# Kernel tuning notes

Hardware: AMD Instinct MI355X
Metric: run time of the kernel (lower is better)

## Reference

```python
import jax, jax.numpy as jnp
import numpy as np

B, L, H, V = 256, 4096, 64, 64
LN_EPS = 1e-5


def setup_inputs() -> dict:
    key = jax.random.key(0)
    ks = jax.random.split(key, 12)
    s = 1.0 / np.sqrt(H)
    return {
        "seq": jax.random.randint(ks[0], (B, L), 0, V),
        "embed_W": jax.random.normal(ks[1], (V, H), jnp.float32),
        "ff_w1": jax.random.normal(ks[2], (H, 2 * H), jnp.float32) * s,
        "ff_b1": jnp.zeros((2 * H,), jnp.float32),
        "ff_w2": jax.random.normal(ks[3], (2 * H, H), jnp.float32) * s,
        "ff_b2": jnp.zeros((H,), jnp.float32),
        "ln_w": jnp.ones((H,), jnp.float32),
        "ln_b": jnp.zeros((H,), jnp.float32),
        "read_w": jax.random.normal(ks[4], (H, H), jnp.float32) * s,
        "read_b": jnp.zeros((H,), jnp.float32),
        "out_w": jax.random.normal(ks[5], (H, V), jnp.float32) * s,
        "out_b": jnp.zeros((V,), jnp.float32),
    }


def _layer_norm(x, w, b):
    mu = jnp.mean(x, axis=-1, keepdims=True)
    var = jnp.mean(jnp.square(x - mu), axis=-1, keepdims=True)
    return (x - mu) * jax.lax.rsqrt(var + LN_EPS) * w + b


def reference(seq, embed_W, ff_w1, ff_b1, ff_w2, ff_b2, ln_w, ln_b,
              read_w, read_b, out_w, out_b):
    h = embed_W[seq]  # (B, L, H)
    ff = jax.nn.relu(h @ ff_w1 + ff_b1) @ ff_w2 + ff_b2
    h = _layer_norm(h + ff, ln_w, ln_b)

    def step(M, k):  # M: (B,H,H), k: (B,H)
        v_pred = jnp.einsum('bij,bj->bi', M, k)
        denom = jnp.sum(k * k, axis=-1, keepdims=True) + 1e-6
        dv = k - v_pred / denom
        M = M + dv[:, :, None] * k[:, None, :]  # rank-1 delta write
        return M, None

    ks = jnp.swapaxes(h[:, :-1, :], 0, 1)  # (L-1, B, H)
    M0 = jnp.zeros((h.shape[0], h.shape[-1], h.shape[-1]), h.dtype)
    M, _ = jax.lax.scan(step, M0, ks)

    q = h[:, -1, :]
    ctx = jnp.einsum('bij,bj->bi', M, q)
    return (ctx @ read_w + read_b) @ out_w + out_b  # (B, V)
```

## Files before the change

### kernel.cpp

```cpp
#include <hip/hip_runtime.h>
#include <hip/hip_bf16.h>

#define LN_EPS 1e-5f

static __device__ __forceinline__ float readlane_f(float v, int lane) {
    return __int_as_float(__builtin_amdgcn_readlane(__float_as_int(v), lane));
}
static __device__ __forceinline__ void writelane_f(int& dst, float val, int lane_imm) {
    asm volatile("v_writelane_b32 %0, %1, %2"
                 : "+v"(dst)
                 : "s"(__float_as_int(val)), "i"(lane_imm));
}

__global__ __launch_bounds__(64) void build_keys(
    const float* __restrict__ embed,
    const float* __restrict__ w1,
    const float* __restrict__ b1,
    const float* __restrict__ w2,
    const float* __restrict__ b2,
    const float* __restrict__ lnw,
    const float* __restrict__ lnb,
    float* __restrict__ keytab)
{
    const int v = blockIdx.x, lane = threadIdx.x;
    __shared__ float se[64];
    __shared__ float sh[128];
    se[lane] = embed[v * 64 + lane];
    __syncthreads();
    float h0 = b1[lane];
    float h1 = b1[lane + 64];
    #pragma unroll 8
    for (int i = 0; i < 64; ++i) {
        float e = se[i];
        h0 = fmaf(e, w1[i * 128 + lane], h0);
        h1 = fmaf(e, w1[i * 128 + lane + 64], h1);
    }
    sh[lane]      = fmaxf(h0, 0.f);
    sh[lane + 64] = fmaxf(h1, 0.f);
    __syncthreads();
    float acc = b2[lane];
    #pragma unroll 8
    for (int j = 0; j < 128; ++j)
        acc = fmaf(sh[j], w2[j * 64 + lane], acc);
    float pre = se[lane] + acc;
    float sum = pre;
    #pragma unroll
    for (int off = 32; off >= 1; off >>= 1) sum += __shfl_xor(sum, off, 64);
    float mu  = sum * (1.f / 64.f);
    float dev = pre - mu;
    float sq  = dev * dev;
    #pragma unroll
    for (int off = 32; off >= 1; off >>= 1) sq += __shfl_xor(sq, off, 64);
    float var = sq * (1.f / 64.f);
    float key = dev * (1.f / sqrtf(var + LN_EPS)) * lnw[lane] + lnb[lane];
    keytab[v * 64 + lane] = key;
}

__global__ __launch_bounds__(64) void build_tables(
    const float* __restrict__ keytab,
    const float* __restrict__ read_w,
    const float* __restrict__ read_b,
    const float* __restrict__ out_w,
    const float* __restrict__ out_b,
    float* __restrict__ Gg,
    float* __restrict__ GhatN,
    float* __restrict__ Wc,
    float* __restrict__ biasv)
{
    const int w = blockIdx.x, lane = threadIdx.x;
    __shared__ float sk[64 * 65];
    __shared__ float srw[64];
    #pragma unroll 8
    for (int r = 0; r < 64; ++r) sk[r * 65 + lane] = keytab[r * 64 + lane];
    srw[lane] = read_w[w * 64 + lane];
    __syncthreads();
    float g = 0.f;
    #pragma unroll 8
    for (int i = 0; i < 64; ++i)
        g = fmaf(sk[w * 65 + i], sk[lane * 65 + i], g);
    float gww  = readlane_f(g, w);
    float beta = 1.f / (gww + 1e-6f);
    Gg[w * 64 + lane]    = g;
    GhatN[w * 64 + lane] = -(beta * g);
    float acc = 0.f;
    #pragma unroll 8
    for (int j = 0; j < 64; ++j)
        acc = fmaf(srw[j], out_w[j * 64 + lane], acc);
    Wc[w * 64 + lane] = acc;
    if (w == 0) {
        float bacc = out_b[lane];
        #pragma unroll 8
        for (int j = 0; j < 64; ++j)
            bacc = fmaf(read_b[j], out_w[j * 64 + lane], bacc);
        biasv[lane] = bacc;
    }
}

__global__ __launch_bounds__(64) void delta_scan(
    const int*   __restrict__ seq,
    const float* __restrict__ Gg,
    const float* __restrict__ GhatN,
    const float* __restrict__ keytab,
    const float* __restrict__ Wc,
    const float* __restrict__ biasv,
    float* __restrict__ out)
{
    const int lane = threadIdx.x;
    const int b    = blockIdx.x;
    __shared__ float sG[64 * 64];
    __shared__ float sc[64];
    __shared__ float sCtx[64];
    #pragma unroll 8
    for (int r = 0; r < 64; ++r) sG[r * 64 + lane] = GhatN[r * 64 + lane];
    sc[lane] = 0.f;
    const int* seqb = seq + (size_t)b * 4096;
    float d = Gg[seqb[4095] * 64 + lane];
    __syncthreads();

    int vS = 0;
    int vcur = seqb[64 * 63 + lane];
    int   wq[21];
    float q_[21];
    #pragma unroll
    for (int s = 0; s < 21; ++s) {
        wq[s] = __builtin_amdgcn_readlane(vcur, 62 - s);
        q_[s] = sG[wq[s] * 64 + lane];
    }

    #pragma unroll 1
    for (int blk = 64; blk >= 0; --blk) {
        int vnext = (blk > 0) ? seqb[(blk - 1) * 63 + lane] : vcur;
        #pragma unroll
        for (int j = 62; j >= 0; --j) {
            const int slot = (62 - j) % 21;
            const int jl   = j - 21;
            int   w0 = wq[slot];
            float p  = readlane_f(d, w0);
            d = fmaf(p, q_[slot], d);
            writelane_f(vS, p, j);
            int wn = (jl >= 0) ? __builtin_amdgcn_readlane(vcur, jl)
                               : __builtin_amdgcn_readlane(vnext, jl + 63);
            wq[slot] = wn;
            q_[slot] = sG[wn * 64 + lane];
        }
        atomicAdd(&sc[vcur & 63], __int_as_float(vS));
        vS = 0;
        vcur = vnext;
    }
    __syncthreads();

    float ctx = 0.f;
    #pragma unroll 8
    for (int v = 0; v < 64; ++v)
        ctx = fmaf(sc[v], keytab[v * 64 + lane], ctx);
    sCtx[lane] = ctx;
    __syncthreads();
    float o = biasv[lane];
    #pragma unroll 8
    for (int i = 0; i < 64; ++i)
        o = fmaf(sCtx[i], Wc[i * 64 + lane], o);
    out[(size_t)b * 64 + lane] = o;
}

extern "C" void kernel_launch(void* const* d_in, const int* in_sizes, int n_in,
                              void* d_out, int out_size, void* d_ws, size_t ws_size,
                              hipStream_t stream) {
    const int*   seq    = (const int*)d_in[0];
    const float* embed  = (const float*)d_in[1];
    const float* ff_w1  = (const float*)d_in[2];
    const float* ff_b1  = (const float*)d_in[3];
    const float* ff_w2  = (const float*)d_in[4];
    const float* ff_b2  = (const float*)d_in[5];
    const float* ln_w   = (const float*)d_in[6];
    const float* ln_b   = (const float*)d_in[7];
    const float* read_w = (const float*)d_in[8];
    const float* read_b = (const float*)d_in[9];
    const float* out_w  = (const float*)d_in[10];
    const float* out_b  = (const float*)d_in[11];
    float* out = (float*)d_out;

    float* wsf    = (float*)d_ws;
    float* keytab = wsf;
    float* Gg     = wsf + 4096;
    float* GhatN  = wsf + 8192;
    float* Wc     = wsf + 12288;
    float* biasv  = wsf + 16384;

    build_keys<<<64, 64, 0, stream>>>(embed, ff_w1, ff_b1, ff_w2, ff_b2, ln_w, ln_b, keytab);
    build_tables<<<64, 64, 0, stream>>>(keytab, read_w, read_b, out_w, out_b,
                                        Gg, GhatN, Wc, biasv);
    delta_scan<<<256, 64, 0, stream>>>(seq, Gg, GhatN, keytab, Wc, biasv, out);
}
```

Baseline: 167.3 us.

## Pair scan steps algebraically and read Gram rows from global memory instead of LDS

The serial delta-scan recurrence now processes two steps per iteration. The second step's readlane is computed from the first step's value plus a precomputed cross term, which shortens the dependent chain of readlane and fma per step. The shared-memory copy of the normalized Gram table is removed, and rows are fetched straight from global memory (likely L1/L2-resident). This trades the LDS preload and its latency for global loads, and adds one extra readlane plus readfirstlane per pair.

```diff
diff --git a/kernel.cpp b/kernel.cpp
--- a/kernel.cpp
+++ b/kernel.cpp
@@ -10,6 +10,12 @@
     asm volatile("v_writelane_b32 %0, %1, %2"
                  : "+v"(dst)
                  : "s"(__float_as_int(val)), "i"(lane_imm));
+}
+static __device__ __forceinline__ void writelane_fu(int& dst, float val, int lane_imm) {
+    int sval = __builtin_amdgcn_readfirstlane(__float_as_int(val));
+    asm volatile("v_writelane_b32 %0, %1, %2"
+                 : "+v"(dst)
+                 : "s"(sval), "i"(lane_imm));
 }
 
 __global__ __launch_bounds__(64) void build_keys(
@@ -107,11 +113,8 @@
 {
     const int lane = threadIdx.x;
     const int b    = blockIdx.x;
-    __shared__ float sG[64 * 64];
     __shared__ float sc[64];
     __shared__ float sCtx[64];
-    #pragma unroll 8
-    for (int r = 0; r < 64; ++r) sG[r * 64 + lane] = GhatN[r * 64 + lane];
     sc[lane] = 0.f;
     const int* seqb = seq + (size_t)b * 4096;
     float d = Gg[seqb[4095] * 64 + lane];
@@ -124,24 +127,41 @@
     #pragma unroll
     for (int s = 0; s < 21; ++s) {
         wq[s] = __builtin_amdgcn_readlane(vcur, 62 - s);
-        q_[s] = sG[wq[s] * 64 + lane];
+        q_[s] = GhatN[wq[s] * 64 + lane];
     }
 
     #pragma unroll 1
     for (int blk = 64; blk >= 0; --blk) {
         int vnext = (blk > 0) ? seqb[(blk - 1) * 63 + lane] : vcur;
         #pragma unroll
-        for (int j = 62; j >= 0; --j) {
-            const int slot = (62 - j) % 21;
-            const int jl   = j - 21;
-            int   w0 = wq[slot];
-            float p  = readlane_f(d, w0);
-            d = fmaf(p, q_[slot], d);
-            writelane_f(vS, p, j);
-            int wn = (jl >= 0) ? __builtin_amdgcn_readlane(vcur, jl)
-                               : __builtin_amdgcn_readlane(vnext, jl + 63);
-            wq[slot] = wn;
-            q_[slot] = sG[wn * 64 + lane];
+        for (int j = 62; j >= 2; j -= 2) {
+            const int s0 = (62 - j) % 21;
+            const int s1 = (63 - j) % 21;
+            const int w0 = wq[s0], w1 = wq[s1];
+            float g0 = readlane_f(d, w0);
+            float g1 = readlane_f(d, w1);
+            float al = readlane_f(q_[s0], w1);
+            float c0 = fmaf(al, q_[s1], q_[s0]);
+            d = fmaf(g0, c0, d);
+            d = fmaf(g1, q_[s1], d);
+            writelane_f(vS, g0, j);
+            float s1v = fmaf(al, g0, g1);
+            writelane_fu(vS, s1v, j - 1);
+            const int jl0 = j - 21, jl1 = j - 22;
+            int wn0 = (jl0 >= 0) ? __builtin_amdgcn_readlane(vcur, jl0)
+                                 : __builtin_amdgcn_readlane(vnext, jl0 + 63);
+            int wn1 = (jl1 >= 0) ? __builtin_amdgcn_readlane(vcur, jl1)
+                                 : __builtin_amdgcn_readlane(vnext, jl1 + 63);
+            wq[s0] = wn0; q_[s0] = GhatN[wn0 * 64 + lane];
+            wq[s1] = wn1; q_[s1] = GhatN[wn1 * 64 + lane];
+        }
+        {
+            const int w0 = wq[20];
+            float g0 = readlane_f(d, w0);
+            d = fmaf(g0, q_[20], d);
+            writelane_f(vS, g0, 0);
+            int wn0 = __builtin_amdgcn_readlane(vnext, 42);
+            wq[20] = wn0; q_[20] = GhatN[wn0 * 64 + lane];
         }
         atomicAdd(&sc[vcur & 63], __int_as_float(vS));
         vS = 0;
```

Result: slower. 203.7 us (+21.8%).
